# Kernel optimization log

Hardware: AMD Instinct MI355X
Metric: run time of the kernel (lower is better)

Reference implementation:

```python
import jax, jax.numpy as jnp
import numpy as np

B, S, D, H = 4, 2048, 1024, 16
HD = D // H  # head_dim = 64


def setup_inputs() -> dict:
    key = jax.random.key(0)
    k_x, k_m, k_wi, k_bi, k_wo, k_bo = jax.random.split(key, 6)
    x = jax.random.normal(k_x, (B, S, D), dtype=jnp.float32)
    mask = jax.random.randint(k_m, (B, S), 0, 2, dtype=jnp.int32)
    # Keras Dense: kernel shape (in, out), glorot-ish scale; bias zeros-ish (random small here)
    w_in = jax.random.normal(k_wi, (D, 3 * D), dtype=jnp.float32) * (1.0 / np.sqrt(D))
    b_in = jax.random.normal(k_bi, (3 * D,), dtype=jnp.float32) * 0.02
    w_out = jax.random.normal(k_wo, (D, D), dtype=jnp.float32) * (1.0 / np.sqrt(D))
    b_out = jax.random.normal(k_bo, (D,), dtype=jnp.float32) * 0.02
    return {"x": x, "w_in": w_in, "b_in": b_in, "w_out": w_out, "b_out": b_out, "mask": mask}


def reference(x, w_in, b_in, w_out, b_out, mask):
    b, s, _ = x.shape
    scale = jnp.asarray(HD ** (-0.5), dtype=x.dtype)
    qkv = x @ w_in + b_in                              # (B, S, 3D)
    qkv = qkv.reshape(b, s, 3, H, HD).transpose(2, 0, 3, 1, 4)  # (3, B, H, S, HD)
    q, k, v = qkv[0], qkv[1], qkv[2]
    q = q * scale
    attn = jnp.einsum("bhqd,bhkd->bhqk", q, k)         # (B, H, S, S)
    neg_inf = jnp.asarray(float("-inf"), dtype=attn.dtype)
    attn_mask = jnp.where(mask[:, None, None, :] > 0, jnp.zeros((), attn.dtype), neg_inf)
    attn = jax.nn.softmax(attn + attn_mask, axis=-1)
    out = jnp.einsum("bhqk,bhkd->bhqd", attn, v)        # (B, H, S, HD)
    out = out.transpose(0, 2, 1, 3).reshape(b, s, D)
    return out @ w_out + b_out
```

## Files before the change

kernel.cpp:

```cpp
#include <hip/hip_runtime.h>

#define B_  4
#define S_  2048
#define D_  1024
#define H_  16
#define HD_ 64
#define BH_ (B_*H_)
#define QSCALE 0.18033688f

typedef _Float16 h16;
typedef _Float16 h4 __attribute__((ext_vector_type(4)));
typedef _Float16 h8 __attribute__((ext_vector_type(8)));
typedef float    f32x4 __attribute__((ext_vector_type(4)));

#define EXP2(x) __builtin_amdgcn_exp2f(x)

__device__ __forceinline__ void gload16(const h16* g, h16* l) {
  __builtin_amdgcn_global_load_lds(
      (const __attribute__((address_space(1))) unsigned int*)g,
      (__attribute__((address_space(3))) unsigned int*)l, 16, 0, 0);
}

__global__ __launch_bounds__(256)
void prep_k(const float* __restrict__ x, const float* __restrict__ w_in,
            const float* __restrict__ b_in, const int* __restrict__ mask,
            h16* __restrict__ xc, h16* __restrict__ WinT,
            h16* __restrict__ binc, int* __restrict__ posmap,
            int* __restrict__ nvalid, int* __restrict__ invmap) {
  __shared__ __align__(16) char smem[2212];
  int blk = blockIdx.x;
  int t = threadIdx.x;
  if (blk < 4) {
    int* partial = (int*)smem;
    int b = blk;
    const int* mb = mask + b * S_;
    int base = t * 8;
    int loc[8], cnt = 0;
#pragma unroll
    for (int j = 0; j < 8; j++) { loc[j] = cnt; cnt += (mb[base + j] != 0); }
    partial[t] = cnt;
    __syncthreads();
    for (int off = 1; off < 256; off <<= 1) {
      int v = (t >= off) ? partial[t - off] : 0;
      __syncthreads();
      partial[t] += v;
      __syncthreads();
    }
    int excl = (t == 0) ? 0 : partial[t - 1];
#pragma unroll
    for (int j = 0; j < 8; j++) {
      if (mb[base + j] != 0) {
        int pos = excl + loc[j];
        posmap[b * S_ + base + j] = pos;
        invmap[b * S_ + pos] = base + j;
      } else {
        posmap[b * S_ + base + j] = -1;
      }
    }
    if (t == 255) nvalid[b] = partial[255];
  } else if (blk < 6) {
    int idx = ((blk - 4) * 256 + t) * 8;
    if (idx + 8 <= 3 * D_) {
      float4 f0 = *(const float4*)(b_in + idx);
      float4 f1 = *(const float4*)(b_in + idx + 4);
      h16 tmp[8] = {(h16)f0.x, (h16)f0.y, (h16)f0.z, (h16)f0.w,
                    (h16)f1.x, (h16)f1.y, (h16)f1.z, (h16)f1.w};
      *(h8*)(binc + idx) = *(h8*)tmp;
    }
  } else if (blk < 4102) {
    int idx = ((blk - 6) * 256 + t) * 8;
    float4 f0 = *(const float4*)(x + idx);
    float4 f1 = *(const float4*)(x + idx + 4);
    h16 tmp[8] = {(h16)f0.x, (h16)f0.y, (h16)f0.z, (h16)f0.w,
                  (h16)f1.x, (h16)f1.y, (h16)f1.z, (h16)f1.w};
    *(h8*)(xc + idx) = *(h8*)tmp;
  } else {
    typedef h16 row33[33];
    row33* tile = (row33*)smem;
    int idx = blk - 4102;
    int bx = (idx % 96) * 32, by = (idx / 96) * 32;
    int tx = t & 31, ty = t >> 5;
    const int C = 3 * D_, R = D_;
#pragma unroll
    for (int i = 0; i < 32; i += 8)
      tile[ty + i][tx] = (h16)w_in[(size_t)(by + ty + i) * C + bx + tx];
    __syncthreads();
#pragma unroll
    for (int i = 0; i < 32; i += 8)
      WinT[(size_t)(bx + ty + i) * R + by + tx] = tile[tx][ty + i];
  }
}

__global__ __launch_bounds__(256)
void post_k(const float* __restrict__ w_out, const float* __restrict__ b_out,
            h16* __restrict__ WouT, h16* __restrict__ boutc) {
  __shared__ h16 tile[32][33];
  int blk = blockIdx.x;
  int t = threadIdx.x;
  if (blk < 1024) {
    int bx = (blk % 32) * 32, by = (blk / 32) * 32;
    int tx = t & 31, ty = t >> 5;
#pragma unroll
    for (int i = 0; i < 32; i += 8)
      tile[ty + i][tx] = (h16)w_out[(size_t)(by + ty + i) * D_ + bx + tx];
    __syncthreads();
#pragma unroll
    for (int i = 0; i < 32; i += 8)
      WouT[(size_t)(bx + ty + i) * D_ + by + tx] = tile[tx][ty + i];
  } else {
    int idx = t * 4;
    if (idx < D_) {
      float4 f = *(const float4*)(b_out + idx);
      h16 tmp[4] = {(h16)f.x, (h16)f.y, (h16)f.z, (h16)f.w};
      *(h4*)(boutc + idx) = *(h4*)tmp;
    }
  }
}

__global__ __launch_bounds__(256)
void gemm_q(const h16* __restrict__ A, const h16* __restrict__ BT,
            const h16* __restrict__ bias, h16* __restrict__ outQ) {
  const int K = D_;
  const int tid  = threadIdx.x;
  const int lane = tid & 63;
  const int w    = tid >> 6;
  const int quad = lane >> 4;
  const int l16  = lane & 15;
  const int m0   = blockIdx.x * 128;
  const int n0   = blockIdx.y * 128;

  __shared__ alignas(16) h16 As[128 * 64];
  __shared__ alignas(16) h16 Bs[128 * 64];

  const f32x4 zero = {0.f, 0.f, 0.f, 0.f};
  f32x4 acc[4][4];
#pragma unroll
  for (int i = 0; i < 4; i++)
#pragma unroll
    for (int j = 0; j < 4; j++) acc[i][j] = zero;

  const int wm = (w >> 1) * 64;
  const int wn = (w & 1) * 64;
  const int sw = l16 & 7;

  for (int kt = 0; kt < K; kt += 64) {
#pragma unroll
    for (int p = 0; p < 4; p++) {
      int c   = w * 256 + p * 64 + lane;
      int row = c >> 3;
      int cc  = (c & 7) ^ (row & 7);
      gload16(&A[(size_t)(m0 + row) * K + kt + cc * 8],
              &As[(w * 256 + p * 64) * 8]);
      gload16(&BT[(size_t)(n0 + row) * K + kt + cc * 8],
              &Bs[(w * 256 + p * 64) * 8]);
    }
    __syncthreads();
#pragma unroll
    for (int kk = 0; kk < 2; kk++) {
      h8 af[4], bfr[4];
#pragma unroll
      for (int i = 0; i < 4; i++)
        af[i] = *(const h8*)(&As[(wm + i * 16 + l16) * 64 +
                                 ((kk * 4 + quad) ^ sw) * 8]);
#pragma unroll
      for (int j = 0; j < 4; j++)
        bfr[j] = *(const h8*)(&Bs[(wn + j * 16 + l16) * 64 +
                                  ((kk * 4 + quad) ^ sw) * 8]);
#pragma unroll
      for (int i = 0; i < 4; i++)
#pragma unroll
        for (int j = 0; j < 4; j++)
          acc[i][j] = __builtin_amdgcn_mfma_f32_16x16x32_f16(af[i], bfr[j],
                                                             acc[i][j], 0, 0, 0);
    }
    __syncthreads();
  }

#pragma unroll
  for (int i = 0; i < 4; i++) {
#pragma unroll
    for (int j = 0; j < 4; j++) {
      int n = n0 + wn + j * 16 + l16;
      float bv = (float)bias[n];
      int h  = (n >> 6) & 15;
      int hd = n & 63;
#pragma unroll
      for (int r = 0; r < 4; r++) {
        int m = m0 + wm + i * 16 + quad * 4 + r;
        int b = m >> 11;
        int s = m & 2047;
        float v = acc[i][j][r] + bv;
        outQ[(((size_t)(b * 16 + h)) * S_ + s) * HD_ + hd] = (h16)(v * QSCALE);
      }
    }
  }
}

__global__ __launch_bounds__(256)
void gemm_kv(const h16* __restrict__ xc, const h16* __restrict__ BT,
             const h16* __restrict__ bias, const int* __restrict__ invmap,
             const int* __restrict__ nvalid,
             h16* __restrict__ Kc, h16* __restrict__ Vtc) {
  const int bb = blockIdx.z;
  const int nv = nvalid[bb];
  const int m0 = blockIdx.x * 128;
  if (m0 >= nv) return;
  const int K = D_;
  const int n0 = blockIdx.y * 128;
  const int tid  = threadIdx.x;
  const int lane = tid & 63;
  const int w    = tid >> 6;
  const int quad = lane >> 4;
  const int l16  = lane & 15;
  const int wm = (w >> 1) * 64;
  const int wn = (w & 1) * 64;
  const int sw = l16 & 7;

  const h16* Ab = xc + (size_t)bb * S_ * D_;
  const int* im = invmap + bb * S_;

  int srow[4];
#pragma unroll
  for (int p = 0; p < 4; p++) {
    int c   = w * 256 + p * 64 + lane;
    int row = c >> 3;
    int m   = m0 + row;
    srow[p] = im[m < nv ? m : nv - 1];
  }

  __shared__ alignas(16) h16 As[128 * 64];
  __shared__ alignas(16) h16 Bs[128 * 64];

  const f32x4 zero = {0.f, 0.f, 0.f, 0.f};
  f32x4 acc[4][4];
#pragma unroll
  for (int i = 0; i < 4; i++)
#pragma unroll
    for (int j = 0; j < 4; j++) acc[i][j] = zero;

  for (int kt = 0; kt < K; kt += 64) {
#pragma unroll
    for (int p = 0; p < 4; p++) {
      int c   = w * 256 + p * 64 + lane;
      int row = c >> 3;
      int cc  = (c & 7) ^ (row & 7);
      gload16(&Ab[(size_t)srow[p] * K + kt + cc * 8],
              &As[(w * 256 + p * 64) * 8]);
      gload16(&BT[(size_t)(n0 + row) * K + kt + cc * 8],
              &Bs[(w * 256 + p * 64) * 8]);
    }
    __syncthreads();
#pragma unroll
    for (int kk = 0; kk < 2; kk++) {
      h8 af[4], bfr[4];
#pragma unroll
      for (int i = 0; i < 4; i++)
        af[i] = *(const h8*)(&As[(wm + i * 16 + l16) * 64 +
                                 ((kk * 4 + quad) ^ sw) * 8]);
#pragma unroll
      for (int j = 0; j < 4; j++)
        bfr[j] = *(const h8*)(&Bs[(wn + j * 16 + l16) * 64 +
                                  ((kk * 4 + quad) ^ sw) * 8]);
#pragma unroll
      for (int i = 0; i < 4; i++)
#pragma unroll
        for (int j = 0; j < 4; j++)
          acc[i][j] = __builtin_amdgcn_mfma_f32_16x16x32_f16(af[i], bfr[j],
                                                             acc[i][j], 0, 0, 0);
    }
    __syncthreads();
  }

#pragma unroll
  for (int i = 0; i < 4; i++) {
#pragma unroll
    for (int j = 0; j < 4; j++) {
      int n = n0 + wn + j * 16 + l16;
      float bv = (float)bias[n];
      int which = n >> 10;
      int h  = (n >> 6) & 15;
      int hd = n & 63;
#pragma unroll
      for (int r = 0; r < 4; r++) {
        int m = m0 + wm + i * 16 + quad * 4 + r;
        if (m < nv) {
          float v = acc[i][j][r] + bv;
          if (which == 0)
            Kc[(((size_t)(bb * 16 + h)) * S_ + m) * HD_ + hd] = (h16)v;
          else
            Vtc[(((size_t)(bb * 16 + h)) * HD_ + hd) * S_ + m] = (h16)v;
        }
      }
    }
  }
}

__global__ __launch_bounds__(256)
void gemm_bt1(const h16* __restrict__ A, const h16* __restrict__ BT,
              const h16* __restrict__ bias, float* __restrict__ out,
              int M, int N, int K) {
  const int tid  = threadIdx.x;
  const int lane = tid & 63;
  const int w    = tid >> 6;
  const int quad = lane >> 4;
  const int l16  = lane & 15;
  const int m0   = blockIdx.x * 128;
  const int n0   = blockIdx.y * 128;

  __shared__ alignas(16) h16 As[128 * 64];
  __shared__ alignas(16) h16 Bs[128 * 64];

  const f32x4 zero = {0.f, 0.f, 0.f, 0.f};
  f32x4 acc[4][4];
#pragma unroll
  for (int i = 0; i < 4; i++)
#pragma unroll
    for (int j = 0; j < 4; j++) acc[i][j] = zero;

  const int wm = (w >> 1) * 64;
  const int wn = (w & 1) * 64;
  const int sw = l16 & 7;

  for (int kt = 0; kt < K; kt += 64) {
#pragma unroll
    for (int p = 0; p < 4; p++) {
      int c   = w * 256 + p * 64 + lane;
      int row = c >> 3;
      int cc  = (c & 7) ^ (row & 7);
      gload16(&A[(size_t)(m0 + row) * K + kt + cc * 8],
              &As[(w * 256 + p * 64) * 8]);
      gload16(&BT[(size_t)(n0 + row) * K + kt + cc * 8],
              &Bs[(w * 256 + p * 64) * 8]);
    }
    __syncthreads();
#pragma unroll
    for (int kk = 0; kk < 2; kk++) {
      h8 af[4], bfr[4];
#pragma unroll
      for (int i = 0; i < 4; i++)
        af[i] = *(const h8*)(&As[(wm + i * 16 + l16) * 64 +
                                 ((kk * 4 + quad) ^ sw) * 8]);
#pragma unroll
      for (int j = 0; j < 4; j++)
        bfr[j] = *(const h8*)(&Bs[(wn + j * 16 + l16) * 64 +
                                  ((kk * 4 + quad) ^ sw) * 8]);
#pragma unroll
      for (int i = 0; i < 4; i++)
#pragma unroll
        for (int j = 0; j < 4; j++)
          acc[i][j] = __builtin_amdgcn_mfma_f32_16x16x32_f16(af[i], bfr[j],
                                                             acc[i][j], 0, 0, 0);
    }
    __syncthreads();
  }

#pragma unroll
  for (int i = 0; i < 4; i++) {
#pragma unroll
    for (int j = 0; j < 4; j++) {
      int n = n0 + wn + j * 16 + l16;
      float bv = (float)bias[n];
#pragma unroll
      for (int r = 0; r < 4; r++) {
        int m = m0 + wm + i * 16 + quad * 4 + r;
        out[(size_t)m * N + n] = acc[i][j][r] + bv;
      }
    }
  }
}

__global__ __launch_bounds__(256)
void attn_k(const h16* __restrict__ Q, const h16* __restrict__ Kc,
            const h16* __restrict__ Vtc, const int* __restrict__ nvalid,
            h16* __restrict__ out) {
  const int tid  = threadIdx.x;
  const int lane = tid & 63;
  const int w    = tid >> 6;
  const int quad = lane >> 4;
  const int l16  = lane & 15;
  const int bh   = blockIdx.y;
  const int b    = bh >> 4, h = bh & 15;
  const int q0   = blockIdx.x * 64 + w * 16;
  const int nv   = nvalid[b];
  const int sw   = l16 & 7;

  const h16* Qh = Q   + (size_t)bh * S_ * HD_;
  const h16* Kh = Kc  + (size_t)bh * S_ * HD_;
  const h16* Vh = Vtc + (size_t)bh * HD_ * S_;

  __shared__ alignas(16) h16 Ks[64 * 64];
  __shared__ alignas(16) h16 Vs[64 * 64];
  __shared__ alignas(16) h16 Pb[4][16 * 72];

  h8 bq[2];
#pragma unroll
  for (int ks = 0; ks < 2; ks++)
    bq[ks] = *(const h8*)(&Qh[(size_t)(q0 + l16) * 64 + ks * 32 + quad * 8]);

  const f32x4 zero = {0.f, 0.f, 0.f, 0.f};
  f32x4 oacc[4];
#pragma unroll
  for (int j = 0; j < 4; j++) oacc[j] = zero;
  float mst = -1e30f, lst = 0.f;

  for (int kb = 0; kb < nv; kb += 64) {
    __syncthreads();
#pragma unroll
    for (int p = 0; p < 2; p++) {
      int c   = w * 128 + p * 64 + lane;
      int row = c >> 3;
      int cc  = (c & 7) ^ (row & 7);
      gload16(&Kh[(size_t)(kb + row) * 64 + cc * 8],
              &Ks[(w * 128 + p * 64) * 8]);
      gload16(&Vh[(size_t)row * S_ + kb + cc * 8],
              &Vs[(w * 128 + p * 64) * 8]);
    }
    __syncthreads();

    f32x4 st[4];
#pragma unroll
    for (int kh = 0; kh < 4; kh++) {
      h8 ak0 = *(const h8*)(&Ks[(kh * 16 + l16) * 64 + (quad ^ sw) * 8]);
      h8 ak1 = *(const h8*)(&Ks[(kh * 16 + l16) * 64 + ((quad + 4) ^ sw) * 8]);
      f32x4 s = zero;
      s = __builtin_amdgcn_mfma_f32_16x16x32_f16(ak0, bq[0], s, 0, 0, 0);
      s = __builtin_amdgcn_mfma_f32_16x16x32_f16(ak1, bq[1], s, 0, 0, 0);
      st[kh] = s;
    }
    if (kb + 64 > nv) {
#pragma unroll
      for (int kh = 0; kh < 4; kh++)
#pragma unroll
        for (int r = 0; r < 4; r++)
          if (kb + kh * 16 + quad * 4 + r >= nv) st[kh][r] = -1e30f;
    }

    float mx = -1e30f;
#pragma unroll
    for (int kh = 0; kh < 4; kh++)
#pragma unroll
      for (int r = 0; r < 4; r++) mx = fmaxf(mx, st[kh][r]);
    mx = fmaxf(mx, __shfl_xor(mx, 16, 64));
    mx = fmaxf(mx, __shfl_xor(mx, 32, 64));
    float mnew = fmaxf(mst, mx);
    float alpha = EXP2(mst - mnew);
    float p[4][4], rs = 0.f;
#pragma unroll
    for (int kh = 0; kh < 4; kh++)
#pragma unroll
      for (int r = 0; r < 4; r++) {
        p[kh][r] = EXP2(st[kh][r] - mnew);
        rs += p[kh][r];
      }
    rs += __shfl_xor(rs, 16, 64);
    rs += __shfl_xor(rs, 32, 64);
    lst = lst * alpha + rs;
    mst = mnew;

    float al[4];
#pragma unroll
    for (int r = 0; r < 4; r++) al[r] = __shfl(alpha, quad * 4 + r, 64);
#pragma unroll
    for (int j = 0; j < 4; j++)
#pragma unroll
      for (int r = 0; r < 4; r++) oacc[j][r] *= al[r];

    h16* pb = Pb[w];
#pragma unroll
    for (int kh = 0; kh < 4; kh++) {
      h4 pk = {(h16)p[kh][0], (h16)p[kh][1], (h16)p[kh][2], (h16)p[kh][3]};
      *(h4*)(&pb[l16 * 72 + kh * 16 + quad * 4]) = pk;
    }
    h8 pa0 = *(const h8*)(&pb[l16 * 72 + quad * 8]);
    h8 pa1 = *(const h8*)(&pb[l16 * 72 + 32 + quad * 8]);

#pragma unroll
    for (int j = 0; j < 4; j++) {
      h8 bv0 = *(const h8*)(&Vs[(j * 16 + l16) * 64 + (quad ^ sw) * 8]);
      h8 bv1 = *(const h8*)(&Vs[(j * 16 + l16) * 64 + ((quad + 4) ^ sw) * 8]);
      oacc[j] = __builtin_amdgcn_mfma_f32_16x16x32_f16(pa0, bv0, oacc[j], 0, 0, 0);
      oacc[j] = __builtin_amdgcn_mfma_f32_16x16x32_f16(pa1, bv1, oacc[j], 0, 0, 0);
    }
  }

  float ls[4];
#pragma unroll
  for (int r = 0; r < 4; r++) ls[r] = __shfl(lst, quad * 4 + r, 64);
#pragma unroll
  for (int j = 0; j < 4; j++)
#pragma unroll
    for (int r = 0; r < 4; r++) {
      int row = q0 + quad * 4 + r;
      float v = oacc[j][r] / ls[r];
      out[((size_t)(b * S_ + row)) * D_ + h * 64 + j * 16 + l16] = (h16)v;
    }
}

extern "C" void kernel_launch(void* const* d_in, const int* in_sizes, int n_in,
                              void* d_out, int out_size, void* d_ws,
                              size_t ws_size, hipStream_t stream) {
  const float* x     = (const float*)d_in[0];
  const float* w_in  = (const float*)d_in[1];
  const float* b_in  = (const float*)d_in[2];
  const float* w_out = (const float*)d_in[3];
  const float* b_out = (const float*)d_in[4];
  const int*   mask  = (const int*)d_in[5];

  const size_t NT = (size_t)BH_ * S_ * HD_;
  h16* ws    = (h16*)d_ws;
  h16* Qb    = ws;
  h16* Kcb   = ws + NT;
  h16* Vtcb  = ws + 2 * NT;
  h16* xc    = ws + 3 * NT;
  h16* AOb   = ws + 3 * NT;
  h16* WouT  = Qb;
  h16* boutc = Vtcb;
  h16* WinT  = (h16*)d_out;
  h16* binc  = (h16*)d_out + 3400704;
  int* posmap = (int*)((char*)d_out + 24u * 1024 * 1024);
  int* nvalid = posmap + B_ * S_;
  int* invmap = (int*)((char*)d_out + 25u * 1024 * 1024);

  prep_k<<<7174, 256, 0, stream>>>(x, w_in, b_in, mask, xc, WinT, binc,
                                   posmap, nvalid, invmap);

  gemm_q<<<dim3((B_ * S_) / 128, D_ / 128), 256, 0, stream>>>(
      xc, WinT, binc, Qb);

  gemm_kv<<<dim3(S_ / 128, (2 * D_) / 128, B_), 256, 0, stream>>>(
      xc, WinT + (size_t)D_ * D_, binc + D_, invmap, nvalid, Kcb, Vtcb);

  attn_k<<<dim3(S_ / 64, BH_), 256, 0, stream>>>(Qb, Kcb, Vtcb, nvalid, AOb);

  post_k<<<1025, 256, 0, stream>>>(w_out, b_out, WouT, boutc);

  gemm_bt1<<<dim3((B_ * S_) / 128, D_ / 128), 256, 0, stream>>>(
      AOb, WouT, boutc, (float*)d_out, B_ * S_, D_, D_);
}
```

Before: 284.9 us.

## Double-buffer K/V tiles in attention and skip lazy softmax rescaling

The attention kernel now keeps two LDS buffers for K and V. It issues the async global-to-LDS loads for the next tile before computing on the current one, with one wait and barrier per iteration, so memory latency can overlap the MFMA and softmax work. It also adds a lazy rescale: when no row max in the wave grows by more than 8 (log2 units) over the running max, it keeps the old max and skips the exp and the oacc rescaling. This doubles the K/V LDS footprint, which may cut occupancy. The lazy path lets fp16 probabilities go up to 2^8, which stays in fp16 range.

```diff
diff --git a/kernel.cpp b/kernel.cpp
--- a/kernel.cpp
+++ b/kernel.cpp
@@ -388,8 +388,8 @@
   const h16* Kh = Kc  + (size_t)bh * S_ * HD_;
   const h16* Vh = Vtc + (size_t)bh * HD_ * S_;
 
-  __shared__ alignas(16) h16 Ks[64 * 64];
-  __shared__ alignas(16) h16 Vs[64 * 64];
+  __shared__ alignas(16) h16 Ks[2][64 * 64];
+  __shared__ alignas(16) h16 Vs[2][64 * 64];
   __shared__ alignas(16) h16 Pb[4][16 * 72];
 
   h8 bq[2];
@@ -403,25 +403,49 @@
   for (int j = 0; j < 4; j++) oacc[j] = zero;
   float mst = -1e30f, lst = 0.f;
 
-  for (int kb = 0; kb < nv; kb += 64) {
-    __syncthreads();
+  const int ntiles = (nv + 63) >> 6;
+
+  {
 #pragma unroll
     for (int p = 0; p < 2; p++) {
       int c   = w * 128 + p * 64 + lane;
       int row = c >> 3;
       int cc  = (c & 7) ^ (row & 7);
-      gload16(&Kh[(size_t)(kb + row) * 64 + cc * 8],
-              &Ks[(w * 128 + p * 64) * 8]);
-      gload16(&Vh[(size_t)row * S_ + kb + cc * 8],
-              &Vs[(w * 128 + p * 64) * 8]);
-    }
-    __syncthreads();
+      gload16(&Kh[(size_t)(0 + row) * 64 + cc * 8],
+              &Ks[0][(w * 128 + p * 64) * 8]);
+      gload16(&Vh[(size_t)row * S_ + 0 + cc * 8],
+              &Vs[0][(w * 128 + p * 64) * 8]);
+    }
+    asm volatile("s_waitcnt vmcnt(0)" ::: "memory");
+    __syncthreads();
+  }
+
+  for (int it = 0; it < ntiles; ++it) {
+    const int cur = it & 1;
+    const int kb  = it * 64;
+
+    if (it + 1 < ntiles) {
+      const int kb1 = kb + 64;
+#pragma unroll
+      for (int p = 0; p < 2; p++) {
+        int c   = w * 128 + p * 64 + lane;
+        int row = c >> 3;
+        int cc  = (c & 7) ^ (row & 7);
+        gload16(&Kh[(size_t)(kb1 + row) * 64 + cc * 8],
+                &Ks[cur ^ 1][(w * 128 + p * 64) * 8]);
+        gload16(&Vh[(size_t)row * S_ + kb1 + cc * 8],
+                &Vs[cur ^ 1][(w * 128 + p * 64) * 8]);
+      }
+    }
+
+    const h16* Kb = Ks[cur];
+    const h16* Vb = Vs[cur];
 
     f32x4 st[4];
 #pragma unroll
     for (int kh = 0; kh < 4; kh++) {
-      h8 ak0 = *(const h8*)(&Ks[(kh * 16 + l16) * 64 + (quad ^ sw) * 8]);
-      h8 ak1 = *(const h8*)(&Ks[(kh * 16 + l16) * 64 + ((quad + 4) ^ sw) * 8]);
+      h8 ak0 = *(const h8*)(&Kb[(kh * 16 + l16) * 64 + (quad ^ sw) * 8]);
+      h8 ak1 = *(const h8*)(&Kb[(kh * 16 + l16) * 64 + ((quad + 4) ^ sw) * 8]);
       f32x4 s = zero;
       s = __builtin_amdgcn_mfma_f32_16x16x32_f16(ak0, bq[0], s, 0, 0, 0);
       s = __builtin_amdgcn_mfma_f32_16x16x32_f16(ak1, bq[1], s, 0, 0, 0);
@@ -442,8 +466,10 @@
       for (int r = 0; r < 4; r++) mx = fmaxf(mx, st[kh][r]);
     mx = fmaxf(mx, __shfl_xor(mx, 16, 64));
     mx = fmaxf(mx, __shfl_xor(mx, 32, 64));
-    float mnew = fmaxf(mst, mx);
-    float alpha = EXP2(mst - mnew);
+
+    const bool skip = __all(mx <= mst + 8.0f);
+    float mnew = skip ? mst : fmaxf(mst, mx);
+
     float p[4][4], rs = 0.f;
 #pragma unroll
     for (int kh = 0; kh < 4; kh++)
@@ -454,16 +480,21 @@
       }
     rs += __shfl_xor(rs, 16, 64);
     rs += __shfl_xor(rs, 32, 64);
-    lst = lst * alpha + rs;
-    mst = mnew;
-
-    float al[4];
-#pragma unroll
-    for (int r = 0; r < 4; r++) al[r] = __shfl(alpha, quad * 4 + r, 64);
-#pragma unroll
-    for (int j = 0; j < 4; j++)
-#pragma unroll
-      for (int r = 0; r < 4; r++) oacc[j][r] *= al[r];
+
+    if (skip) {
+      lst += rs;
+    } else {
+      float alpha = EXP2(mst - mnew);
+      lst = lst * alpha + rs;
+      mst = mnew;
+      float al[4];
+#pragma unroll
+      for (int r = 0; r < 4; r++) al[r] = __shfl(alpha, quad * 4 + r, 64);
+#pragma unroll
+      for (int j = 0; j < 4; j++)
+#pragma unroll
+        for (int r = 0; r < 4; r++) oacc[j][r] *= al[r];
+    }
 
     h16* pb = Pb[w];
 #pragma unroll
@@ -476,11 +507,14 @@
 
 #pragma unroll
     for (int j = 0; j < 4; j++) {
-      h8 bv0 = *(const h8*)(&Vs[(j * 16 + l16) * 64 + (quad ^ sw) * 8]);
-      h8 bv1 = *(const h8*)(&Vs[(j * 16 + l16) * 64 + ((quad + 4) ^ sw) * 8]);
+      h8 bv0 = *(const h8*)(&Vb[(j * 16 + l16) * 64 + (quad ^ sw) * 8]);
+      h8 bv1 = *(const h8*)(&Vb[(j * 16 + l16) * 64 + ((quad + 4) ^ sw) * 8]);
       oacc[j] = __builtin_amdgcn_mfma_f32_16x16x32_f16(pa0, bv0, oacc[j], 0, 0, 0);
       oacc[j] = __builtin_amdgcn_mfma_f32_16x16x32_f16(pa1, bv1, oacc[j], 0, 0, 0);
     }
+
+    asm volatile("s_waitcnt vmcnt(0)" ::: "memory");
+    __syncthreads();
   }
 
   float ls[4];
```

New measurement: 284.2 us. No clear change (-0.2%).
